# Performance work log

Hardware: AMD Instinct MI355X
Metric: run time of the kernel (lower is better)

The kernel has to match this reference:

```python
import jax, jax.numpy as jnp
import numpy as np

DIM = 256   # model dim (forced by gate Linear(32,4): d = 32 = DIM//H)
H = 8       # heads (hard-coded by mask.repeat(1,8,1,1))
D = DIM // H
B = 256     # batch
NS = 100    # skeleton tokens (sub-block size)
NQ = 64     # query tokens
N = NS + NQ # 164
NE = 4      # experts
HID = 50    # expert hidden
LN_EPS = 1e-5


def setup_inputs() -> dict:
    key = jax.random.key(0)
    ks = jax.random.split(key, 12)
    s = 0.02
    return {
        "x": jax.random.normal(ks[0], (B, N, DIM), jnp.float32),
        "mask": jax.random.randint(ks[1], (B, N), 0, 2).astype(bool),
        "w_qk_s": jax.random.normal(ks[2], (DIM, 2 * DIM), jnp.float32) * s,
        "w_qk_q": jax.random.normal(ks[3], (DIM, 2 * DIM), jnp.float32) * s,
        "w_v": jax.random.normal(ks[4], (DIM, DIM), jnp.float32) * s,
        "w_gate": jax.random.normal(ks[5], (D, NE), jnp.float32) * s,
        "b_gate": jnp.zeros((NE,), jnp.float32),
        "ln_gamma": jnp.ones((NE,), jnp.float32),
        "ln_beta": jnp.zeros((NE,), jnp.float32),
        "w1": jax.random.normal(ks[6], (NE, NS, HID), jnp.float32) * s,
        "b1": jnp.zeros((NE, HID), jnp.float32),
        "w2": jax.random.normal(ks[7], (NE, HID, NS), jnp.float32) * s,
        "b2": jnp.zeros((NE, NS), jnp.float32),
        "w_out": jax.random.normal(ks[8], (DIM, DIM), jnp.float32) * s,
        "b_out": jnp.zeros((DIM,), jnp.float32),
    }


def reference(x, mask, w_qk_s, w_qk_q, w_v, w_gate, b_gate, ln_gamma, ln_beta,
              w1, b1, w2, b2, w_out, b_out):
    b, n, dim = x.shape
    scale = dim ** -0.5  # scale_with_head=False -> dim**-0.5

    def to_heads(t):  # (b, m, H*D) -> (b, H, m, D)
        return t.reshape(b, -1, H, D).transpose(0, 2, 1, 3)

    # separate qk projections for skeleton (first 100) vs query (last 64) tokens
    q_s, k_s = jnp.split(x[:, :NS] @ w_qk_s, 2, axis=-1)
    q_q, k_q = jnp.split(x[:, NS:] @ w_qk_q, 2, axis=-1)
    q = jnp.concatenate([to_heads(q_s), to_heads(q_q)], axis=2)  # (b,H,N,D)
    k = jnp.concatenate([to_heads(k_s), to_heads(k_q)], axis=2)
    v = to_heads(x @ w_v)

    # gates: RAW reshape of x (b,n,H*D) -> (b,H,n,D) (memory reinterpretation,
    # as in torch x.reshape), detached, sliced to first 100 'rows'
    gx = jax.lax.stop_gradient(x).reshape(b, H, n, D)[:, :, :NS, :]
    g = gx @ w_gate + b_gate                              # (b,H,100,4)
    mu = g.mean(-1, keepdims=True)
    var = g.var(-1, keepdims=True)
    g = (g - mu) / jnp.sqrt(var + LN_EPS) * ln_gamma + ln_beta
    gates = jax.nn.softmax(g, axis=-1)                    # (b,H,100,4)

    dots = jnp.einsum('bhid,bhjd->bhij', q, k) * scale    # (b,H,N,N)
    mask_value = -jnp.finfo(dots.dtype).max
    dots = jnp.where(mask[:, None, None, :], mask_value, dots)

    # soft-MoE over the 100x100 sub-block (experts applied along key axis)
    attn_q = dots[:, :, :NS, :NS]                         # (b,H,100,100)
    h1 = jax.nn.relu(jnp.einsum('bhij,ejk->bheik', jax.nn.relu(attn_q), w1)
                     + b1[:, None, :])                    # (b,H,4,100,50)
    eo = jax.nn.relu(jnp.einsum('bheik,ekj->bheij', h1, w2)
                     + b2[:, None, :])                    # (b,H,4,100,100)
    moes = jnp.einsum('bheij,bhie->bhij', eo, gates)      # (b,H,100,100)

    dots = dots.at[:, :, :NS, :NS].add(moes)
    attn = jax.nn.softmax(dots, axis=-1)
    out = jnp.einsum('bhij,bhjd->bhid', attn, v)          # (b,H,N,D)
    out = out.transpose(0, 2, 1, 3).reshape(b, n, dim)
    return out @ w_out + b_out
```

## Files before the change

### kernel.cpp

```cpp
#include <hip/hip_runtime.h>

typedef __bf16 bf16x8 __attribute__((ext_vector_type(8)));
typedef __bf16 bf16x4 __attribute__((ext_vector_type(4)));
typedef float  f32x4  __attribute__((ext_vector_type(4)));

__device__ __forceinline__ bf16x8 ldb8(const __bf16* p) {
    return *reinterpret_cast<const bf16x8*>(p);
}
__device__ __forceinline__ bf16x8 zero8() {
    bf16x8 z;
    #pragma unroll
    for (int i = 0; i < 8; i++) z[i] = (__bf16)0.f;
    return z;
}
__device__ __forceinline__ __bf16 ldw(const void* p, int i, int m) {
    return m ? (__bf16)((const float*)p)[i] : ((const __bf16*)p)[i];
}
__device__ __forceinline__ bf16x8 ldx8(const void* p, size_t ei, int m) {
    if (m) {
        const float* f = (const float*)p + ei;
        f32x4 a = *reinterpret_cast<const f32x4*>(f);
        f32x4 b = *reinterpret_cast<const f32x4*>(f + 4);
        bf16x8 r;
        #pragma unroll
        for (int u = 0; u < 4; u++) { r[u] = (__bf16)a[u]; r[4 + u] = (__bf16)b[u]; }
        return r;
    }
    return ldb8((const __bf16*)p + ei);
}

__global__ __launch_bounds__(256) void prep_kernel(
    const void* x, const void* mask,
    const void* wqks, const void* wqkq, const void* wv, const void* w1,
    const void* w2, const void* wout, const void* wg, const void* bg,
    const void* lng, const void* lnb, const void* b1, const void* b2,
    const void* bout, int* modes, unsigned* maskb,
    __bf16* __restrict__ Wts, __bf16* __restrict__ Wtq,
    __bf16* __restrict__ w1t, __bf16* __restrict__ w2t,
    __bf16* __restrict__ wot, __bf16* __restrict__ wsm)
{
    __shared__ int sbad;
    const int t = threadIdx.x, bid = blockIdx.x;
    if (t == 0) sbad = 0;
    __syncthreads();
    {
        const unsigned int* xw = (const unsigned int*)x;
        int bad = 0;
        for (int i = t; i < 2048; i += 256) {
            unsigned int w = xw[i];
            unsigned int el = (w >> 7) & 0xFF, eh = (w >> 23) & 0xFF;
            if (el >= 0x94 || el == 0xFF) bad++;
            if (eh >= 0x94 || eh == 0xFF) bad++;
        }
        if (bad) atomicAdd(&sbad, bad);
    }
    __syncthreads();
    const int m = (sbad > 64) ? 1 : 0;

    if (bid >= 1268) {
        __shared__ int v32bad, v16bad;
        __shared__ unsigned mb[24];
        const int mbid = bid - 1268;
        if (t == 0) { v32bad = 0; v16bad = 0; }
        if (t < 24) mb[t] = ((t % 6) == 5) ? 0xFFFFFFF0u : 0u;
        __syncthreads();
        const unsigned int* mw = (const unsigned int*)mask;
        int b32 = 0, b16 = 0;
        for (int i = t; i < 10496; i += 256) {
            unsigned int w = mw[i];
            if (!(w == 0u || w == 1u || w == 0x3F800000u)) b32++;
            unsigned int h0 = w & 0xFFFFu, h1 = w >> 16;
            if (!(h0 == 0u || h0 == 1u || h0 == 0x3F80u)) b16++;
            if (!(h1 == 0u || h1 == 1u || h1 == 0x3F80u)) b16++;
        }
        if (b32) atomicAdd(&v32bad, b32);
        if (b16) atomicAdd(&v16bad, b16);
        __syncthreads();
        const int mmode = (v32bad == 0) ? 0 : ((v16bad == 0) ? 2 : 1);
        if (mbid == 0 && t == 0) { modes[0] = m; modes[1] = mmode; }
        const int lo = mbid * 656;
        for (int i2 = t; i2 < 656; i2 += 256) {
            int i = lo + i2;
            int val;
            if (mmode == 0)      val = (((const int*)mask)[i] != 0);
            else if (mmode == 2) val = (((const unsigned short*)mask)[i] != 0);
            else                 val = (((const unsigned char*)mask)[i] != 0);
            if (val) {
                int ib = i2 / 164, jb = i2 - ib * 164;
                atomicOr(&mb[ib * 6 + (jb >> 5)], 1u << (jb & 31));
            }
        }
        __syncthreads();
        if (t < 24) maskb[mbid * 24 + t] = mb[t];
        return;
    }

    int i = bid * 256 + t;
    if (i < 196608) {
        int n = i >> 8, k = i & 255;
        __bf16 vs, vq;
        if (n < 512) { vs = ldw(wqks, k * 512 + n, m); vq = ldw(wqkq, k * 512 + n, m); }
        else         { vs = ldw(wv, k * 256 + (n - 512), m); vq = vs; }
        Wts[i] = vs; Wtq[i] = vq;
        return;
    }
    i -= 196608;
    if (i < 32768) {
        int e = i >> 13, r = i & 8191, n = r >> 7, k = r & 127;
        __bf16 v = (__bf16)0.f;
        if (n < 50) {
            if (k < 100)       v = ldw(w1, (e * 100 + k) * 50 + n, m);
            else if (k == 100) v = ldw(b1, e * 50 + n, m);
        }
        w1t[i] = v;
        return;
    }
    i -= 32768;
    if (i < 28672) {
        int e = i / 7168, r = i % 7168, n = r >> 6, k = r & 63;
        __bf16 v = (__bf16)0.f;
        if (n < 100) {
            if (k < 50)       v = ldw(w2, (e * 50 + k) * 100 + n, m);
            else if (k == 50) v = ldw(b2, e * 100 + n, m);
        }
        w2t[i] = v;
        return;
    }
    i -= 28672;
    if (i < 65536) {
        int n = i >> 8, k = i & 255;
        wot[i] = ldw(wout, k * 256 + n, m);
        return;
    }
    i -= 65536;
    if (i < 996) {
        __bf16 v;
        if (i < 128)      v = ldw(wg, i, m);
        else if (i < 132) v = ldw(bg, i - 128, m);
        else if (i < 136) v = ldw(lng, i - 132, m);
        else if (i < 140) v = ldw(lnb, i - 136, m);
        else if (i < 340) v = ldw(b1, i - 140, m);
        else if (i < 740) v = ldw(b2, i - 340, m);
        else              v = ldw(bout, i - 740, m);
        wsm[i] = v;
    }
}

__global__ __launch_bounds__(256, 3) void qkv_kernel(
    const void* __restrict__ x, const __bf16* __restrict__ Wts,
    const __bf16* __restrict__ Wtq, const __bf16* __restrict__ wsm,
    const int* __restrict__ modes,
    __bf16* __restrict__ q, __bf16* __restrict__ k, __bf16* __restrict__ vt,
    float* __restrict__ gates)
{
    __shared__ __bf16 xs[32][264];
    __shared__ float wgf[128];
    __shared__ float gcst[12];
    const int m = modes[0];
    const int b = blockIdx.y;
    const int mt = blockIdx.x >> 1;
    const int half = blockIdx.x & 1;
    const __bf16* Wt = (mt < 4) ? Wts : Wtq;
    const int rbase = (mt < 4) ? mt * 32 : 100 + (mt - 4) * 32;
    const int tid = threadIdx.x;

    if (tid < 128) wgf[tid] = (float)wsm[tid];
    if (tid < 12)  gcst[tid] = (float)wsm[128 + tid];
    for (int c = tid; c < 1024; c += 256) {
        int row = c >> 5, part = c & 31;
        bf16x8 val = ldx8(x, ((size_t)b * 164 + rbase + row) * 256 + part * 8, m);
        *reinterpret_cast<bf16x8*>(&xs[row][part * 8]) = val;
    }
    __syncthreads();

    const int w = tid >> 6, l = tid & 63, lr = l & 15, lc = l >> 4;
    f32x4 acc[2][6];
    #pragma unroll
    for (int ms = 0; ms < 2; ms++)
        #pragma unroll
        for (int nt = 0; nt < 6; nt++) acc[ms][nt] = (f32x4){0.f, 0.f, 0.f, 0.f};

    #pragma unroll
    for (int kt = 0; kt < 8; kt++) {
        bf16x8 a0 = ldb8(&xs[lr][kt * 32 + lc * 8]);
        bf16x8 a1 = ldb8(&xs[16 + lr][kt * 32 + lc * 8]);
        #pragma unroll
        for (int nt = 0; nt < 6; nt++) {
            bf16x8 bb = ldb8(Wt + (size_t)(half * 384 + w * 96 + nt * 16 + lr) * 256 + kt * 32 + lc * 8);
            acc[0][nt] = __builtin_amdgcn_mfma_f32_16x16x32_bf16(a0, bb, acc[0][nt], 0, 0, 0);
            acc[1][nt] = __builtin_amdgcn_mfma_f32_16x16x32_bf16(a1, bb, acc[1][nt], 0, 0, 0);
        }
    }
    #pragma unroll
    for (int ms = 0; ms < 2; ms++) {
        #pragma unroll
        for (int nt = 0; nt < 6; nt++) {
            int c = half * 384 + w * 96 + nt * 16 + lr;
            int i0 = rbase + ms * 16 + lc * 4;
            if (c < 512) {
                __bf16* dst; int ch;
                if (c < 256) { dst = q; ch = c; }
                else         { dst = k; ch = c - 256; }
                int hh = ch >> 5, d = ch & 31;
                #pragma unroll
                for (int r = 0; r < 4; r++) {
                    int i = i0 + r;
                    if (mt >= 4 || i < 100)
                        dst[(((size_t)b * 8 + hh) * 164 + i) * 32 + d] = (__bf16)acc[ms][nt][r];
                }
            } else {
                int ch = c - 512, hh = ch >> 5, d = ch & 31;
                if (mt >= 4 || i0 < 100) {
                    bf16x4 pv;
                    #pragma unroll
                    for (int r = 0; r < 4; r++) pv[r] = (__bf16)acc[ms][nt][r];
                    *reinterpret_cast<bf16x4*>(&vt[((size_t)(b * 8 + hh) * 32 + d) * 176 + i0]) = pv;
                }
            }
        }
    }

    if ((tid >> 7) == half) {
        int jg = rbase * 8 + tid;
        int h = jg / 164;
        int j = jg - h * 164;
        if (j < 100) {
            const __bf16* xp = &xs[tid >> 3][(tid & 7) * 32];
            float g[4] = {gcst[0], gcst[1], gcst[2], gcst[3]};
            #pragma unroll
            for (int p = 0; p < 4; p++) {
                bf16x8 xv = ldb8(xp + p * 8);
                #pragma unroll
                for (int u = 0; u < 8; u++) {
                    float f = (float)xv[u];
                    #pragma unroll
                    for (int e = 0; e < 4; e++) g[e] += f * wgf[(p * 8 + u) * 4 + e];
                }
            }
            float mu = 0.25f * (g[0] + g[1] + g[2] + g[3]);
            float var = 0.25f * ((g[0]-mu)*(g[0]-mu) + (g[1]-mu)*(g[1]-mu) +
                                 (g[2]-mu)*(g[2]-mu) + (g[3]-mu)*(g[3]-mu));
            float is = rsqrtf(var + 1e-5f);
            float mx = -3.0e38f;
            #pragma unroll
            for (int e = 0; e < 4; e++) {
                g[e] = (g[e] - mu) * is * gcst[4 + e] + gcst[8 + e];
                mx = fmaxf(mx, g[e]);
            }
            float s = 0.f;
            #pragma unroll
            for (int e = 0; e < 4; e++) { g[e] = __expf(g[e] - mx); s += g[e]; }
            float inv = 1.f / s;
            float4 gv = make_float4(g[0]*inv, g[1]*inv, g[2]*inv, g[3]*inv);
            *reinterpret_cast<float4*>(&gates[((size_t)(b * 8 + h) * 100 + j) * 4]) = gv;
        }
    }
}

__global__ __launch_bounds__(256, 4) void attn_kernel(
    const __bf16* __restrict__ qg, const __bf16* __restrict__ kg,
    const __bf16* __restrict__ vtg, const float* __restrict__ gatesg,
    const unsigned* __restrict__ maskbg, const __bf16* __restrict__ w1t,
    const __bf16* __restrict__ w2t, __bf16* __restrict__ ohg)
{
    __shared__ __align__(16) __bf16 lds[19712];
    const int flat = blockIdx.x;
    const int xcd = flat & 7, j5 = flat >> 3;
    const int bh = ((j5 & 255) << 3) | xcd;
    const int rt = j5 >> 8;
    const int b = bh >> 3, tid = threadIdx.x;
    const int w = tid >> 6, l = tid & 63, lr = l & 15, lc = l >> 4;
    const int m0 = w * 16;
    const int WB  = 6400 + w * 3328;
    const int H1B = WB + 2176;
    const bool moe_wave = (rt * 64 + m0) < 100;

    const __bf16* vtb = vtg + (size_t)bh * 32 * 176;
    bf16x8 vv0, vv1, vv2;
    {
        int c = tid;
        int row = c / 24, j0 = (c - row * 24) * 8;
        if (j0 < 164) {
            vv0 = ldb8(vtb + row * 176 + j0);
            if (j0 == 160) { vv0[4] = (__bf16)0.f; vv0[5] = (__bf16)0.f; vv0[6] = (__bf16)0.f; vv0[7] = (__bf16)0.f; }
        } else vv0 = zero8();
    }
    {
        int c = tid + 256;
        int row = c / 24, j0 = (c - row * 24) * 8;
        if (j0 < 164) {
            vv1 = ldb8(vtb + row * 176 + j0);
            if (j0 == 160) { vv1[4] = (__bf16)0.f; vv1[5] = (__bf16)0.f; vv1[6] = (__bf16)0.f; vv1[7] = (__bf16)0.f; }
        } else vv1 = zero8();
    }
    {
        int c = tid + 512;
        int row = c / 24, j0 = (c - row * 24) * 8;
        if (j0 < 164) {
            vv2 = ldb8(vtb + row * 176 + j0);
            if (j0 == 160) { vv2[4] = (__bf16)0.f; vv2[5] = (__bf16)0.f; vv2[6] = (__bf16)0.f; vv2[7] = (__bf16)0.f; }
        } else vv2 = zero8();
    }

    const unsigned* mbp = maskbg + b * 6;
    unsigned mbits = 0;
    #pragma unroll
    for (int nt = 0; nt < 11; nt++)
        mbits |= ((mbp[nt >> 1] >> (((nt & 1) << 4) + lr)) & 1u) << nt;
    int qrow = rt * 64 + m0 + lr; if (qrow > 163) qrow = 163;
    bf16x8 afq = ldb8(qg + ((size_t)bh * 164 + qrow) * 32 + lc * 8);

    const __bf16* kbase = kg + (size_t)bh * 164 * 32;
    f32x4 raw[11];
    #pragma unroll
    for (int nt = 0; nt < 11; nt++) {
        int krow = nt * 16 + lr; if (krow > 163) krow = 163;
        bf16x8 kb = ldb8(kbase + (size_t)krow * 32 + lc * 8);
        f32x4 acc = {0.f, 0.f, 0.f, 0.f};
        acc = __builtin_amdgcn_mfma_f32_16x16x32_bf16(afq, kb, acc, 0, 0, 0);
        bool bad = (mbits >> nt) & 1;
        #pragma unroll
        for (int r = 0; r < 4; r++)
            raw[nt][r] = bad ? -1e30f : acc[r] * 0.0625f;
    }

    {
        int c = tid;
        int row = c / 24, j0 = (c - row * 24) * 8;
        *reinterpret_cast<bf16x8*>(&lds[row * 200 + (j0 ^ ((row & 7) << 3))]) = vv0;
        c = tid + 256;
        row = c / 24; j0 = (c - row * 24) * 8;
        *reinterpret_cast<bf16x8*>(&lds[row * 200 + (j0 ^ ((row & 7) << 3))]) = vv1;
        c = tid + 512;
        row = c / 24; j0 = (c - row * 24) * 8;
        *reinterpret_cast<bf16x8*>(&lds[row * 200 + (j0 ^ ((row & 7) << 3))]) = vv2;
    }

    if (moe_wave) {
        #pragma unroll
        for (int nt = 0; nt < 8; nt++) {
            int j = nt * 16 + lr;
            #pragma unroll
            for (int r = 0; r < 4; r++) {
                float v = raw[nt][r];
                v = (v < 0.f) ? 0.f : v;
                if (j >= 100) v = (j == 100) ? 1.f : 0.f;
                lds[WB + (lc * 4 + r) * 136 + j] = (__bf16)v;
            }
        }
    }

    if (moe_wave) {
        const int gi0 = rt * 64 + m0 + lc * 4;
        bf16x8 sa[4];
        #pragma unroll
        for (int kt = 0; kt < 4; kt++)
            sa[kt] = ldb8(&lds[WB + lr * 136 + kt * 32 + lc * 8]);
        for (int e = 0; e < 4; e++) {
            #pragma unroll
            for (int nt = 0; nt < 4; nt++) {
                f32x4 acc = {0.f, 0.f, 0.f, 0.f};
                __builtin_amdgcn_s_setprio(1);
                #pragma unroll
                for (int kt = 0; kt < 4; kt++) {
                    bf16x8 bb = ldb8(w1t + (size_t)(e * 64 + nt * 16 + lr) * 128 + kt * 32 + lc * 8);
                    acc = __builtin_amdgcn_mfma_f32_16x16x32_bf16(sa[kt], bb, acc, 0, 0, 0);
                }
                __builtin_amdgcn_s_setprio(0);
                int n = nt * 16 + lr;
                #pragma unroll
                for (int r = 0; r < 4; r++) {
                    float v = acc[r];
                    if (v < 0.f) v = 0.f;
                    if (n == 50) v = 1.f;
                    lds[H1B + (lc * 4 + r) * 72 + n] = (__bf16)v;
                }
            }
            bf16x8 ha0 = ldb8(&lds[H1B + lr * 72 + lc * 8]);
            bf16x8 ha1 = ldb8(&lds[H1B + lr * 72 + 32 + lc * 8]);
            float gt[4];
            #pragma unroll
            for (int r = 0; r < 4; r++) {
                int gi = gi0 + r;
                gt[r] = (gi < 100) ? gatesg[((size_t)bh * 100 + gi) * 4 + e] : 0.f;
            }
            #pragma unroll
            for (int nt = 0; nt < 7; nt++) {
                f32x4 acc = {0.f, 0.f, 0.f, 0.f};
                __builtin_amdgcn_s_setprio(1);
                bf16x8 bb0 = ldb8(w2t + (size_t)(e * 112 + nt * 16 + lr) * 64 + lc * 8);
                acc = __builtin_amdgcn_mfma_f32_16x16x32_bf16(ha0, bb0, acc, 0, 0, 0);
                bf16x8 bb1 = ldb8(w2t + (size_t)(e * 112 + nt * 16 + lr) * 64 + 32 + lc * 8);
                acc = __builtin_amdgcn_mfma_f32_16x16x32_bf16(ha1, bb1, acc, 0, 0, 0);
                __builtin_amdgcn_s_setprio(0);
                #pragma unroll
                for (int r = 0; r < 4; r++) {
                    float v = acc[r];
                    if (v < 0.f) v = 0.f;
                    raw[nt][r] += v * gt[r];
                }
            }
        }
    }

    float mx = -3.0e38f;
    #pragma unroll
    for (int nt = 0; nt < 11; nt++)
        #pragma unroll
        for (int r = 0; r < 4; r++) mx = fmaxf(mx, raw[nt][r]);
    const bool fast = __all(mx <= 8.f) && __any(mx > -1e29f);
    float s2v0, s2v1, s2v2, s2v3;
    #pragma unroll
    for (int r = 0; r < 4; r++) {
        float m2 = 8.f;
        if (!fast) {
            m2 = raw[0][r];
            #pragma unroll
            for (int nt = 1; nt < 11; nt++) m2 = fmaxf(m2, raw[nt][r]);
            m2 = fmaxf(m2, __shfl_xor(m2, 1, 64));
            m2 = fmaxf(m2, __shfl_xor(m2, 2, 64));
            m2 = fmaxf(m2, __shfl_xor(m2, 4, 64));
            m2 = fmaxf(m2, __shfl_xor(m2, 8, 64));
        }
        float s2 = 0.f;
        #pragma unroll
        for (int nt = 0; nt < 11; nt++) {
            float ev = __expf(raw[nt][r] - m2);
            raw[nt][r] = ev;
            s2 += ev;
        }
        s2 += __shfl_xor(s2, 1, 64);
        s2 += __shfl_xor(s2, 2, 64);
        s2 += __shfl_xor(s2, 4, 64);
        s2 += __shfl_xor(s2, 8, 64);
        if (r == 0) s2v0 = s2; else if (r == 1) s2v1 = s2;
        else if (r == 2) s2v2 = s2; else s2v3 = s2;
        const int rowp = lc * 4 + r;
        const int key = (rowp & 7) << 3;
        #pragma unroll
        for (int nt = 0; nt < 11; nt++)
            lds[WB + rowp * 200 + ((nt * 16 + lr) ^ key)] = (__bf16)raw[nt][r];
        lds[WB + rowp * 200 + ((176 + lr) ^ key)] = (__bf16)0.f;
    }
    float vsel = (lr & 3) == 0 ? s2v0 : (lr & 3) == 1 ? s2v1
               : (lr & 3) == 2 ? s2v2 : s2v3;
    float s2row = __shfl(vsel, (lr >> 2) * 16 + lr, 64);
    float invr = (s2row > 0.f) ? (1.f / s2row) : 0.f;
    __syncthreads();

    int gi = rt * 64 + m0 + lr;
    #pragma unroll
    for (int nt = 0; nt < 2; nt++) {
        f32x4 acc = {0.f, 0.f, 0.f, 0.f};
        __builtin_amdgcn_s_setprio(1);
        #pragma unroll
        for (int kt = 0; kt < 6; kt++) {
            int rowv = nt * 16 + lr;
            int col = kt * 32 + lc * 8;
            bf16x8 va = ldb8(&lds[rowv * 200 + (col ^ ((rowv & 7) << 3))]);
            bf16x8 pb = ldb8(&lds[WB + lr * 200 + (col ^ ((lr & 7) << 3))]);
            acc = __builtin_amdgcn_mfma_f32_16x16x32_bf16(va, pb, acc, 0, 0, 0);
        }
        __builtin_amdgcn_s_setprio(0);
        if (gi < 164) {
            bf16x4 ov;
            #pragma unroll
            for (int r = 0; r < 4; r++) ov[r] = (__bf16)(acc[r] * invr);
            *reinterpret_cast<bf16x4*>(&ohg[((size_t)bh * 164 + gi) * 32 + nt * 16 + lc * 4]) = ov;
        }
    }
}

__global__ __launch_bounds__(256) void outproj_kernel(
    const __bf16* __restrict__ oh, const __bf16* __restrict__ wot,
    const __bf16* __restrict__ wsm, float* __restrict__ out)
{
    const __bf16* bout = wsm + 740;
    const int b = blockIdx.y;
    const int mt = blockIdx.x >> 2;
    const int ntile = blockIdx.x & 3;
    const int tid = threadIdx.x;
    const int w = tid >> 6, l = tid & 63, lr = l & 15, lc = l >> 4;
    int row = mt * 64 + w * 16 + lr; if (row > 163) row = 163;
    f32x4 acc[4];
    #pragma unroll
    for (int nt = 0; nt < 4; nt++) acc[nt] = (f32x4){0.f, 0.f, 0.f, 0.f};
    #pragma unroll
    for (int kt = 0; kt < 8; kt++) {
        bf16x8 a = ldb8(oh + (((size_t)b * 8 + kt) * 164 + row) * 32 + lc * 8);
        #pragma unroll
        for (int nt = 0; nt < 4; nt++) {
            bf16x8 bb = ldb8(wot + (size_t)(ntile * 64 + nt * 16 + lr) * 256 + kt * 32 + lc * 8);
            acc[nt] = __builtin_amdgcn_mfma_f32_16x16x32_bf16(a, bb, acc[nt], 0, 0, 0);
        }
    }
    #pragma unroll
    for (int nt = 0; nt < 4; nt++) {
        int n = ntile * 64 + nt * 16 + lr;
        float bias = (float)bout[n];
        #pragma unroll
        for (int r = 0; r < 4; r++) {
            int i = mt * 64 + w * 16 + lc * 4 + r;
            if (i < 164)
                out[((size_t)b * 164 + i) * 256 + n] = acc[nt][r] + bias;
        }
    }
}

extern "C" void kernel_launch(void* const* d_in, const int* in_sizes, int n_in,
                              void* d_out, int out_size, void* d_ws, size_t ws_size,
                              hipStream_t stream) {
    const void* x      = d_in[0];
    const void* mask   = d_in[1];
    const void* w_qk_s = d_in[2];
    const void* w_qk_q = d_in[3];
    const void* w_v    = d_in[4];
    const void* w_gate = d_in[5];
    const void* b_gate = d_in[6];
    const void* ln_g   = d_in[7];
    const void* ln_b   = d_in[8];
    const void* w1     = d_in[9];
    const void* b1     = d_in[10];
    const void* w2     = d_in[11];
    const void* b2     = d_in[12];
    const void* w_out  = d_in[13];
    const void* b_out  = d_in[14];
    float* out = (float*)d_out;

    char* ws = (char*)d_ws;
    size_t off = 0;
    auto nextp = [&](size_t bytes) {
        char* p = ws + off;
        off += (bytes + 255) & ~(size_t)255;
        return p;
    };
    const size_t QKV_ELEMS = (size_t)256 * 8 * 164 * 32;
    const size_t VT_ELEMS  = (size_t)256 * 8 * 32 * 176;
    int*      modes  = (int*)nextp(64);
    unsigned* maskb  = (unsigned*)nextp((size_t)256 * 6 * 4);
    __bf16* qws  = (__bf16*)nextp(QKV_ELEMS * 2);
    __bf16* kws  = (__bf16*)nextp(QKV_ELEMS * 2);
    __bf16* vtws = (__bf16*)nextp(VT_ELEMS * 2);
    __bf16* ohws = (__bf16*)nextp(QKV_ELEMS * 2);
    float*  gws  = (float*)nextp((size_t)2048 * 100 * 4 * 4);
    __bf16* Wts  = (__bf16*)nextp(768 * 256 * 2);
    __bf16* Wtq  = (__bf16*)nextp(768 * 256 * 2);
    __bf16* w1t  = (__bf16*)nextp(4 * 64 * 128 * 2);
    __bf16* w2t  = (__bf16*)nextp(4 * 112 * 64 * 2);
    __bf16* wot  = (__bf16*)nextp(256 * 256 * 2);
    __bf16* wsm  = (__bf16*)nextp(996 * 2);

    prep_kernel<<<1332, 256, 0, stream>>>(x, mask, w_qk_s, w_qk_q, w_v, w1, w2,
                                          w_out, w_gate, b_gate, ln_g, ln_b, b1,
                                          b2, b_out, modes, maskb,
                                          Wts, Wtq, w1t, w2t, wot, wsm);
    qkv_kernel<<<dim3(12, 256), 256, 0, stream>>>(x, Wts, Wtq, wsm, modes,
                                                  qws, kws, vtws, gws);
    attn_kernel<<<6144, 256, 0, stream>>>(qws, kws, vtws, gws, maskb,
                                          w1t, w2t, ohws);
    outproj_kernel<<<dim3(12, 256), 256, 0, stream>>>(ohws, wot, wsm, out);
}
```

Before: 486.1 us.

## Load V fragments directly from global in attn kernel, drop shared V staging

The attention kernel no longer stages the V^T tile into shared memory. Each wave now loads its V fragments straight from global memory inside the P·V MFMA loop. This shrinks LDS use per block, removes the block-wide barrier and the XOR swizzle on the P scratch, and raises the launch-bounds occupancy hint from 4 to 6 blocks. The trade-off is that each wave re-reads V from global or L2 instead of sharing one cooperative load, so global-load latency now sits in the MFMA loop.

```diff
diff --git a/kernel.cpp b/kernel.cpp
--- a/kernel.cpp
+++ b/kernel.cpp
@@ -257,13 +257,13 @@
     }
 }
 
-__global__ __launch_bounds__(256, 4) void attn_kernel(
+__global__ __launch_bounds__(256, 6) void attn_kernel(
     const __bf16* __restrict__ qg, const __bf16* __restrict__ kg,
     const __bf16* __restrict__ vtg, const float* __restrict__ gatesg,
     const unsigned* __restrict__ maskbg, const __bf16* __restrict__ w1t,
     const __bf16* __restrict__ w2t, __bf16* __restrict__ ohg)
 {
-    __shared__ __align__(16) __bf16 lds[19712];
+    __shared__ __align__(16) __bf16 lds[13312];
     const int flat = blockIdx.x;
     const int xcd = flat & 7, j5 = flat >> 3;
     const int bh = ((j5 & 255) << 3) | xcd;
@@ -271,36 +271,9 @@
     const int b = bh >> 3, tid = threadIdx.x;
     const int w = tid >> 6, l = tid & 63, lr = l & 15, lc = l >> 4;
     const int m0 = w * 16;
-    const int WB  = 6400 + w * 3328;
+    const int WB  = w * 3328;
     const int H1B = WB + 2176;
     const bool moe_wave = (rt * 64 + m0) < 100;
-
-    const __bf16* vtb = vtg + (size_t)bh * 32 * 176;
-    bf16x8 vv0, vv1, vv2;
-    {
-        int c = tid;
-        int row = c / 24, j0 = (c - row * 24) * 8;
-        if (j0 < 164) {
-            vv0 = ldb8(vtb + row * 176 + j0);
-            if (j0 == 160) { vv0[4] = (__bf16)0.f; vv0[5] = (__bf16)0.f; vv0[6] = (__bf16)0.f; vv0[7] = (__bf16)0.f; }
-        } else vv0 = zero8();
-    }
-    {
-        int c = tid + 256;
-        int row = c / 24, j0 = (c - row * 24) * 8;
-        if (j0 < 164) {
-            vv1 = ldb8(vtb + row * 176 + j0);
-            if (j0 == 160) { vv1[4] = (__bf16)0.f; vv1[5] = (__bf16)0.f; vv1[6] = (__bf16)0.f; vv1[7] = (__bf16)0.f; }
-        } else vv1 = zero8();
-    }
-    {
-        int c = tid + 512;
-        int row = c / 24, j0 = (c - row * 24) * 8;
-        if (j0 < 164) {
-            vv2 = ldb8(vtb + row * 176 + j0);
-            if (j0 == 160) { vv2[4] = (__bf16)0.f; vv2[5] = (__bf16)0.f; vv2[6] = (__bf16)0.f; vv2[7] = (__bf16)0.f; }
-        } else vv2 = zero8();
-    }
 
     const unsigned* mbp = maskbg + b * 6;
     unsigned mbits = 0;
@@ -322,18 +295,6 @@
         #pragma unroll
         for (int r = 0; r < 4; r++)
             raw[nt][r] = bad ? -1e30f : acc[r] * 0.0625f;
-    }
-
-    {
-        int c = tid;
-        int row = c / 24, j0 = (c - row * 24) * 8;
-        *reinterpret_cast<bf16x8*>(&lds[row * 200 + (j0 ^ ((row & 7) << 3))]) = vv0;
-        c = tid + 256;
-        row = c / 24; j0 = (c - row * 24) * 8;
-        *reinterpret_cast<bf16x8*>(&lds[row * 200 + (j0 ^ ((row & 7) << 3))]) = vv1;
-        c = tid + 512;
-        row = c / 24; j0 = (c - row * 24) * 8;
-        *reinterpret_cast<bf16x8*>(&lds[row * 200 + (j0 ^ ((row & 7) << 3))]) = vv2;
     }
 
     if (moe_wave) {
@@ -436,29 +397,36 @@
         if (r == 0) s2v0 = s2; else if (r == 1) s2v1 = s2;
         else if (r == 2) s2v2 = s2; else s2v3 = s2;
         const int rowp = lc * 4 + r;
-        const int key = (rowp & 7) << 3;
         #pragma unroll
         for (int nt = 0; nt < 11; nt++)
-            lds[WB + rowp * 200 + ((nt * 16 + lr) ^ key)] = (__bf16)raw[nt][r];
-        lds[WB + rowp * 200 + ((176 + lr) ^ key)] = (__bf16)0.f;
+            lds[WB + rowp * 200 + nt * 16 + lr] = (__bf16)raw[nt][r];
+        lds[WB + rowp * 200 + 176 + lr] = (__bf16)0.f;
     }
     float vsel = (lr & 3) == 0 ? s2v0 : (lr & 3) == 1 ? s2v1
                : (lr & 3) == 2 ? s2v2 : s2v3;
     float s2row = __shfl(vsel, (lr >> 2) * 16 + lr, 64);
     float invr = (s2row > 0.f) ? (1.f / s2row) : 0.f;
-    __syncthreads();
-
+
+    const __bf16* vtb = vtg + (size_t)bh * 32 * 176;
     int gi = rt * 64 + m0 + lr;
     #pragma unroll
     for (int nt = 0; nt < 2; nt++) {
+        const __bf16* vrow = vtb + (size_t)(nt * 16 + lr) * 176;
         f32x4 acc = {0.f, 0.f, 0.f, 0.f};
         __builtin_amdgcn_s_setprio(1);
         #pragma unroll
         for (int kt = 0; kt < 6; kt++) {
-            int rowv = nt * 16 + lr;
-            int col = kt * 32 + lc * 8;
-            bf16x8 va = ldb8(&lds[rowv * 200 + (col ^ ((rowv & 7) << 3))]);
-            bf16x8 pb = ldb8(&lds[WB + lr * 200 + (col ^ ((lr & 7) << 3))]);
+            bf16x8 va;
+            if (kt < 5) {
+                va = ldb8(vrow + kt * 32 + lc * 8);
+            } else if (lc == 0) {
+                va = ldb8(vrow + 160);
+                va[4] = (__bf16)0.f; va[5] = (__bf16)0.f;
+                va[6] = (__bf16)0.f; va[7] = (__bf16)0.f;
+            } else {
+                va = zero8();
+            }
+            bf16x8 pb = ldb8(&lds[WB + lr * 200 + kt * 32 + lc * 8]);
             acc = __builtin_amdgcn_mfma_f32_16x16x32_bf16(va, pb, acc, 0, 0, 0);
         }
         __builtin_amdgcn_s_setprio(0);
```

Measured after the change: 530.7 us. +9.2%, slower.
